# Kernel optimization log

Hardware: AMD Instinct MI355X
Metric: run time of the kernel (lower is better)

Reference implementation:

```python
import jax, jax.numpy as jnp
import numpy as np
import math

N = 4; H = 8; D = 512; DH = D // H; T = 512
MEM = 512; CMEM = 128; RATIO = 4; DFF = 2048; VOCAB = 32000; B = 8
EPS = 1e-5


def _ln(x, g, b):
    mu = x.mean(-1, keepdims=True)
    var = ((x - mu) ** 2).mean(-1, keepdims=True)
    return (x - mu) / jnp.sqrt(var + EPS) * g + b


def _heads(x):
    b, l, _ = x.shape
    return x.reshape(b, l, H, DH).transpose(0, 2, 1, 3)  # [b,h,l,dh]


def _full_attn(q, k, v):
    dots = jnp.einsum('bhid,bhjd->bhij', q, k) * DH ** -0.5
    return jnp.einsum('bhij,bhjd->bhid', jax.nn.softmax(dots, -1), v)


def _pe(t):
    pos = jnp.arange(t, dtype=jnp.float32)[:, None]
    div = jnp.exp(jnp.arange(0, D, 2, dtype=jnp.float32) * (-math.log(10000.0) / D))
    ang = pos * div
    return jnp.stack([jnp.sin(ang), jnp.cos(ang)], axis=-1).reshape(t, D)


def _layer(x, mem, cmem, mask, p):
    (g1, b1, wq, wkv, wo, bo, cw, cb, dw, db, g2, b2, w1, bb1, w2, bb2) = p
    b = x.shape[0]
    y = _ln(x, g1, b1)                       # PreNorm
    q = _heads(y @ wq)
    kv_in = jnp.concatenate([cmem, mem, y], axis=1)
    k, v = jnp.split(kv_in @ wkv, 2, axis=-1)
    k, v = _heads(k), _heads(v)
    dots = jnp.einsum('bhid,bhjd->bhij', q, k) * DH ** -0.5
    mem_tot = mem.shape[1] + cmem.shape[1]
    m2 = mask[:, None, :, None] & mask[:, None, None, :]          # [b,1,t,t]
    fmask = jnp.pad(m2, ((0, 0), (0, 0), (0, 0), (mem_tot, 0)), constant_values=True)
    neg = -jnp.finfo(dots.dtype).max
    dots = jnp.where(fmask, dots, neg)
    out = jnp.einsum('bhij,bhjd->bhid', jax.nn.softmax(dots, -1), v)
    out = out.transpose(0, 2, 1, 3).reshape(b, T, D)
    x = x + out @ wo + bo                    # Residual around attn
    # --- FIFO memory update (t == seq_len, calc_memory) ---
    queue = jnp.concatenate([mem, y], axis=1)        # [b, mem+t, d]
    old_mem = jax.lax.stop_gradient(queue[:, :-MEM]) # detached, len % RATIO == 0
    new_mem = queue[:, -MEM:]
    Lold = old_mem.shape[1]
    seg = old_mem.reshape(b, Lold // RATIO, RATIO, D)
    comp = jnp.einsum('blrd,odr->blo', seg, cw) + cb  # Conv1d k=stride=RATIO
    new_cmem = jnp.concatenate([cmem, comp], axis=1)[:, -CMEM:]
    ck, cv = jnp.split(comp @ wkv, 2, axis=-1)
    ck, cv = _heads(ck), _heads(cv)
    kvlen = k.shape[2]
    start = kvlen - min(mem.shape[1], MEM) - T
    end = kvlen - T
    qd = jax.lax.stop_gradient(q)
    okd = jax.lax.stop_gradient(k[:, :, start:end])
    ovd = jax.lax.stop_gradient(v[:, :, start:end])
    aux = jnp.mean((_full_attn(qd, okd, ovd) - _full_attn(qd, ck, cv)) ** 2)
    recon = jnp.einsum('bld,lm->bmd', comp, dw) + db[None, :, None]  # deconv Linear
    cut = min(recon.shape[1], Lold)
    ae = jnp.mean((old_mem[:, :cut] - recon[:, :cut]) ** 2)
    # --- FF (Residual(PreNorm(FeedForward))) ---
    y2 = _ln(x, g2, b2)
    x = x + jax.nn.gelu(y2 @ w1 + bb1, approximate=False) @ w2 + bb2
    return x, new_mem, new_cmem, aux, ae


def reference(seq, mask, mems, cmems, embed, ln1_g, ln1_b, wq, wkv, wo, bo,
              conv_w, conv_b, deconv_w, deconv_b, ln2_g, ln2_b, w1, b1, w2, b2):
    x = embed[seq] + _pe(seq.shape[1])[None]
    attn_l = jnp.float32(0.0)
    ae_l = jnp.float32(0.0)
    nm, nc = [], []
    for i in range(N):
        p = (ln1_g[i], ln1_b[i], wq[i], wkv[i], wo[i], bo[i], conv_w[i], conv_b[i],
             deconv_w[i], deconv_b[i], ln2_g[i], ln2_b[i], w1[i], b1[i], w2[i], b2[i])
        x, m, c, a, e = _layer(x, mems[i], cmems[i], mask, p)
        nm.append(m); nc.append(c)
        attn_l = attn_l + a; ae_l = ae_l + e
    return x, jnp.stack(nm), jnp.stack(nc), attn_l / N, ae_l / N


def setup_inputs() -> dict:
    key = jax.random.key(0)
    ks = jax.random.split(key, 16)
    s = 0.02
    return {
        'seq': jax.random.randint(ks[0], (B, T), 0, VOCAB),
        'mask': jnp.ones((B, T), dtype=bool),
        'mems': jax.random.normal(ks[1], (N, B, MEM, D), jnp.float32),
        'cmems': jax.random.normal(ks[2], (N, B, CMEM, D), jnp.float32),
        'embed': jax.random.normal(ks[3], (VOCAB, D), jnp.float32) * s,
        'ln1_g': jnp.ones((N, D), jnp.float32),
        'ln1_b': jnp.zeros((N, D), jnp.float32),
        'wq': jax.random.normal(ks[4], (N, D, D), jnp.float32) * s,
        'wkv': jax.random.normal(ks[5], (N, D, 2 * D), jnp.float32) * s,
        'wo': jax.random.normal(ks[6], (N, D, D), jnp.float32) * s,
        'bo': jnp.zeros((N, D), jnp.float32),
        'conv_w': jax.random.normal(ks[7], (N, D, D, RATIO), jnp.float32) * s,
        'conv_b': jnp.zeros((N, D), jnp.float32),
        'deconv_w': jax.random.normal(ks[8], (N, MEM // RATIO, MEM), jnp.float32) * s,
        'deconv_b': jnp.zeros((N, MEM), jnp.float32),
        'ln2_g': jnp.ones((N, D), jnp.float32),
        'ln2_b': jnp.zeros((N, D), jnp.float32),
        'w1': jax.random.normal(ks[9], (N, D, DFF), jnp.float32) * s,
        'b1': jnp.zeros((N, DFF), jnp.float32),
        'w2': jax.random.normal(ks[10], (N, DFF, D), jnp.float32) * s,
        'b2': jnp.zeros((N, D), jnp.float32),
    }
```

## Files before the change

kernel.cpp:

```cpp
#include <hip/hip_runtime.h>
#include <math.h>


#define GBM 128
#define GBN 64
#define GBK 16

template<int EPI>
__global__ __launch_bounds__(256)
void sgemm_k(const float* __restrict__ A, const float* __restrict__ B,
             float* __restrict__ C, const float* __restrict__ bias,
             const float* __restrict__ rbias, const float* __restrict__ ref,
             float* __restrict__ loss,
             int M, int N, int K, int lda, int ldb, int ldc, int ldref,
             long bsA, long bsB, long bsC, long bsRef, int ksplit)
{
    int zb = blockIdx.z;
    int batch = zb / ksplit;
    int ks = zb % ksplit;
    A += (long)batch * bsA;
    B += (long)batch * bsB;
    C += (long)batch * bsC;
    const float* refp = (EPI == 2) ? ref + (long)batch * bsRef : nullptr;

    int m0 = blockIdx.y * GBM;
    int n0 = blockIdx.x * GBN;
    int t = threadIdx.x;
    int tx = t & 15, ty = t >> 4;

    __shared__ float As[GBK][GBM + 4];
    __shared__ float Bs[GBK][GBN];
    __shared__ float red[4];

    float acc[8][4];
#pragma unroll
    for (int i = 0; i < 8; ++i)
#pragma unroll
        for (int j = 0; j < 4; ++j) acc[i][j] = 0.f;

    int arow = t >> 1, acol = (t & 1) * 8;
    int brow = t >> 4, bcol = (t & 15) * 4;

    int kchunk = K / ksplit;
    int kbeg = ks * kchunk, kend = kbeg + kchunk;

    const float* Aptr = A + (long)(m0 + arow) * lda + acol;
    const float* Bptr = B + n0 + bcol;

    for (int k0 = kbeg; k0 < kend; k0 += GBK) {
        float4 a0 = *(const float4*)(Aptr + k0);
        float4 a1 = *(const float4*)(Aptr + k0 + 4);
        float4 b0 = *(const float4*)(Bptr + (long)(k0 + brow) * ldb);
        __syncthreads();
        As[acol + 0][arow] = a0.x;
        As[acol + 1][arow] = a0.y;
        As[acol + 2][arow] = a0.z;
        As[acol + 3][arow] = a0.w;
        As[acol + 4][arow] = a1.x;
        As[acol + 5][arow] = a1.y;
        As[acol + 6][arow] = a1.z;
        As[acol + 7][arow] = a1.w;
        *(float4*)&Bs[brow][bcol] = b0;
        __syncthreads();
#pragma unroll
        for (int kk = 0; kk < GBK; ++kk) {
            float af[8], bf[4];
            *(float4*)&af[0] = *(const float4*)&As[kk][ty * 8];
            *(float4*)&af[4] = *(const float4*)&As[kk][ty * 8 + 4];
            *(float4*)&bf[0] = *(const float4*)&Bs[kk][tx * 4];
#pragma unroll
            for (int i = 0; i < 8; ++i)
#pragma unroll
                for (int j = 0; j < 4; ++j)
                    acc[i][j] = fmaf(af[i], bf[j], acc[i][j]);
        }
    }

    float bv[4] = {0.f, 0.f, 0.f, 0.f};
    if (EPI != 4 && EPI != 2 && bias) *(float4*)bv = *(const float4*)&bias[n0 + tx * 4];

    float lsum = 0.f;
#pragma unroll
    for (int i = 0; i < 8; ++i) {
        int row = m0 + ty * 8 + i;
        float rb = 0.f;
        if (EPI == 2 && rbias) rb = rbias[row];
        float v[4];
#pragma unroll
        for (int j = 0; j < 4; ++j) v[j] = acc[i][j] + bv[j] + rb;
        if (EPI == 0) {
            *(float4*)&C[(long)row * ldc + n0 + tx * 4] = *(float4*)v;
        } else if (EPI == 1) {
            float* cp = &C[(long)row * ldc + n0 + tx * 4];
            float4 old = *(float4*)cp;
            v[0] += old.x; v[1] += old.y; v[2] += old.z; v[3] += old.w;
            *(float4*)cp = *(float4*)v;
        } else if (EPI == 2) {
            const float* rp = &refp[(long)row * ldref + n0 + tx * 4];
#pragma unroll
            for (int j = 0; j < 4; ++j) { float d = v[j] - rp[j]; lsum += d * d; }
        } else if (EPI == 3) {
#pragma unroll
            for (int j = 0; j < 4; ++j)
                v[j] = 0.5f * v[j] * (1.f + erff(v[j] * 0.70710678118654752f));
            *(float4*)&C[(long)row * ldc + n0 + tx * 4] = *(float4*)v;
        } else if (EPI == 4) {
            float* cp = &C[(long)row * ldc + n0 + tx * 4];
#pragma unroll
            for (int j = 0; j < 4; ++j) atomicAdd(cp + j, v[j]);
        }
    }

    if (EPI == 2) {
#pragma unroll
        for (int off = 1; off < 64; off <<= 1) lsum += __shfl_xor(lsum, off);
        if ((t & 63) == 0) red[t >> 6] = lsum;
        __syncthreads();
        if (t == 0) atomicAdd(loss, red[0] + red[1] + red[2] + red[3]);
    }
}

__global__ __launch_bounds__(256)
void attn_k(const float* __restrict__ Q, long qbs,
            const float* __restrict__ K, int ldk, long kbs,
            const float* __restrict__ V, int ldv, long vbs,
            float* __restrict__ O, long obs,
            int Lk, float scale)
{
    int b = blockIdx.z, h = blockIdx.y;
    int lane = threadIdx.x & 63;
    int wv = threadIdx.x >> 6;
    int rw = lane >> 3, g = lane & 7;
    int qrow = blockIdx.x * 32 + wv * 8 + rw;

    const float* qp = Q + (long)b * qbs + (long)qrow * 512 + h * 64 + g * 8;
    float qreg[8];
    *(float4*)&qreg[0] = *(const float4*)qp;
    *(float4*)&qreg[4] = *(const float4*)(qp + 4);

    const float* Kb = K + (long)b * kbs + h * 64;
    const float* Vb = V + (long)b * vbs + h * 64;

    __shared__ float Ks[32][64];
    __shared__ float Vs[32][64];

    int jl = threadIdx.x >> 3;
    int cc = (threadIdx.x & 7) * 8;

    float m = -INFINITY, l = 0.f;
    float acc[8] = {0.f, 0.f, 0.f, 0.f, 0.f, 0.f, 0.f, 0.f};

    for (int j0 = 0; j0 < Lk; j0 += 32) {
        const float* kp = Kb + (long)(j0 + jl) * ldk + cc;
        const float* vp = Vb + (long)(j0 + jl) * ldv + cc;
        float4 k0 = *(const float4*)kp;
        float4 k1 = *(const float4*)(kp + 4);
        float4 v0 = *(const float4*)vp;
        float4 v1 = *(const float4*)(vp + 4);
        __syncthreads();
        *(float4*)&Ks[jl][cc] = k0;
        *(float4*)&Ks[jl][cc + 4] = k1;
        *(float4*)&Vs[jl][cc] = v0;
        *(float4*)&Vs[jl][cc + 4] = v1;
        __syncthreads();
#pragma unroll 8
        for (int jj = 0; jj < 32; ++jj) {
            float4 ka = *(const float4*)&Ks[jj][g * 8];
            float4 kb = *(const float4*)&Ks[jj][g * 8 + 4];
            float p = qreg[0] * ka.x + qreg[1] * ka.y + qreg[2] * ka.z + qreg[3] * ka.w
                    + qreg[4] * kb.x + qreg[5] * kb.y + qreg[6] * kb.z + qreg[7] * kb.w;
            p += __shfl_xor(p, 1);
            p += __shfl_xor(p, 2);
            p += __shfl_xor(p, 4);
            float s = p * scale;
            float mn = fmaxf(m, s);
            float cf = __expf(m - mn);
            float pr = __expf(s - mn);
            l = l * cf + pr;
            m = mn;
            float4 va = *(const float4*)&Vs[jj][g * 8];
            float4 vb = *(const float4*)&Vs[jj][g * 8 + 4];
            acc[0] = acc[0] * cf + pr * va.x;
            acc[1] = acc[1] * cf + pr * va.y;
            acc[2] = acc[2] * cf + pr * va.z;
            acc[3] = acc[3] * cf + pr * va.w;
            acc[4] = acc[4] * cf + pr * vb.x;
            acc[5] = acc[5] * cf + pr * vb.y;
            acc[6] = acc[6] * cf + pr * vb.z;
            acc[7] = acc[7] * cf + pr * vb.w;
        }
    }
    float inv = 1.f / l;
    float* op = O + (long)b * obs + (long)qrow * 512 + h * 64 + g * 8;
    *(float4*)op = make_float4(acc[0] * inv, acc[1] * inv, acc[2] * inv, acc[3] * inv);
    *(float4*)(op + 4) = make_float4(acc[4] * inv, acc[5] * inv, acc[6] * inv, acc[7] * inv);
}

__global__ __launch_bounds__(256)
void ln_k(const float* __restrict__ x, const float* __restrict__ g,
          const float* __restrict__ b, float* __restrict__ y)
{
    int lane = threadIdx.x & 63;
    int row = blockIdx.x * 4 + (threadIdx.x >> 6);
    const float* xr = x + (long)row * 512 + lane * 8;
    float v[8];
    *(float4*)&v[0] = *(const float4*)xr;
    *(float4*)&v[4] = *(const float4*)(xr + 4);
    float s = 0.f, s2 = 0.f;
#pragma unroll
    for (int i = 0; i < 8; ++i) { s += v[i]; s2 += v[i] * v[i]; }
#pragma unroll
    for (int off = 1; off < 64; off <<= 1) {
        s += __shfl_xor(s, off);
        s2 += __shfl_xor(s2, off);
    }
    float mu = s * (1.f / 512.f);
    float var = s2 * (1.f / 512.f) - mu * mu;
    float rstd = rsqrtf(var + 1e-5f);
    float gg[8], bb[8];
    const float* gp = g + lane * 8;
    const float* bp = b + lane * 8;
    *(float4*)&gg[0] = *(const float4*)gp;
    *(float4*)&gg[4] = *(const float4*)(gp + 4);
    *(float4*)&bb[0] = *(const float4*)bp;
    *(float4*)&bb[4] = *(const float4*)(bp + 4);
    float o[8];
#pragma unroll
    for (int i = 0; i < 8; ++i) o[i] = (v[i] - mu) * rstd * gg[i] + bb[i];
    float* yr = y + (long)row * 512 + lane * 8;
    *(float4*)yr = *(float4*)&o[0];
    *(float4*)(yr + 4) = *(float4*)&o[4];
}

__global__ void embed_pe_k(const int* __restrict__ seq, const float* __restrict__ embed,
                           float* __restrict__ X, int total)
{
    int idx = blockIdx.x * 256 + threadIdx.x;
    if (idx >= total) return;
    int d = idx & 511;
    int bt = idx >> 9;
    int tpos = bt & 511;
    int tok = seq[bt];
    float div = __expf(-(float)(d & ~1) * (9.21034037197618f / 512.f));
    float ang = (float)tpos * div;
    float pe = (d & 1) ? cosf(ang) : sinf(ang);
    X[idx] = embed[(long)tok * 512 + d] + pe;
}

__global__ void transpose_cw_k(const float* __restrict__ cw, float* __restrict__ cwT, int total)
{
    int idx = blockIdx.x * 256 + threadIdx.x;
    if (idx >= total) return;
    int r = idx & 3;
    int d = (idx >> 2) & 511;
    int o = (idx >> 11) & 511;
    int L = idx >> 20;
    cwT[(long)L * 1048576 + (long)(r * 512 + d) * 512 + o] = cw[idx];
}
__global__ void transpose_dw_k(const float* __restrict__ dw, float* __restrict__ dwT, int total)
{
    int idx = blockIdx.x * 256 + threadIdx.x;
    if (idx >= total) return;
    int m = idx & 511;
    int j = (idx >> 9) & 127;
    int L = idx >> 16;
    dwT[(long)L * 65536 + m * 128 + j] = dw[idx];
}

__global__ void bias_bcast_k(float* __restrict__ C, const float* __restrict__ bias, int total)
{
    int i = blockIdx.x * 256 + threadIdx.x;
    if (i < total) C[i] = bias[i & 511];
}

__global__ void sqdiff_k(const float* __restrict__ a, const float* __restrict__ b,
                         float* __restrict__ loss, int n4)
{
    __shared__ float red[4];
    int i = blockIdx.x * 256 + threadIdx.x;
    float lsum = 0.f;
    if (i < n4) {
        float4 x = ((const float4*)a)[i];
        float4 y = ((const float4*)b)[i];
        float d0 = x.x - y.x, d1 = x.y - y.y, d2 = x.z - y.z, d3 = x.w - y.w;
        lsum = d0 * d0 + d1 * d1 + d2 * d2 + d3 * d3;
    }
#pragma unroll
    for (int off = 1; off < 64; off <<= 1) lsum += __shfl_xor(lsum, off);
    if ((threadIdx.x & 63) == 0) red[threadIdx.x >> 6] = lsum;
    __syncthreads();
    if (threadIdx.x == 0) atomicAdd(loss, red[0] + red[1] + red[2] + red[3]);
}

__global__ void zero_loss_k(float* loss)
{
    if (threadIdx.x < 8) loss[threadIdx.x] = 0.f;
}

__global__ void finalize_k(const float* __restrict__ loss, float* __restrict__ out)
{
    if (threadIdx.x == 0) out[0] = loss[0] * (1.f / (4.f * 2097152.f));
    if (threadIdx.x == 1) out[1] = loss[1] * (1.f / (4.f * 2097152.f));
}

static void gemm(hipStream_t st, int EPI, const float* A, const float* B, float* C,
                 const float* bias, const float* rbias, const float* ref, float* loss,
                 int M, int N, int K, int lda, int ldb, int ldc, int ldref,
                 long bsA, long bsB, long bsC, long bsRef, int batches, int ksplit)
{
    dim3 g(N / GBN, M / GBM, batches * ksplit), blk(256);
    switch (EPI) {
    case 0: sgemm_k<0><<<g, blk, 0, st>>>(A, B, C, bias, rbias, ref, loss, M, N, K, lda, ldb, ldc, ldref, bsA, bsB, bsC, bsRef, ksplit); break;
    case 1: sgemm_k<1><<<g, blk, 0, st>>>(A, B, C, bias, rbias, ref, loss, M, N, K, lda, ldb, ldc, ldref, bsA, bsB, bsC, bsRef, ksplit); break;
    case 2: sgemm_k<2><<<g, blk, 0, st>>>(A, B, C, bias, rbias, ref, loss, M, N, K, lda, ldb, ldc, ldref, bsA, bsB, bsC, bsRef, ksplit); break;
    case 3: sgemm_k<3><<<g, blk, 0, st>>>(A, B, C, bias, rbias, ref, loss, M, N, K, lda, ldb, ldc, ldref, bsA, bsB, bsC, bsRef, ksplit); break;
    case 4: sgemm_k<4><<<g, blk, 0, st>>>(A, B, C, bias, rbias, ref, loss, M, N, K, lda, ldb, ldc, ldref, bsA, bsB, bsC, bsRef, ksplit); break;
    }
}

static void attn(hipStream_t st, const float* Q, long qbs, const float* K, int ldk, long kbs,
                 const float* V, int ldv, long vbs, float* O, long obs, int Lk)
{
    dim3 g(16, 8, 8), blk(256);
    attn_k<<<g, blk, 0, st>>>(Q, qbs, K, ldk, kbs, V, ldv, vbs, O, obs, Lk, 0.125f);
}

extern "C" void kernel_launch(void* const* d_in, const int* in_sizes, int n_in,
                              void* d_out, int out_size, void* d_ws, size_t ws_size,
                              hipStream_t stream)
{
    const int*   seq     = (const int*)d_in[0];
    const float* mems    = (const float*)d_in[2];
    const float* cmems   = (const float*)d_in[3];
    const float* embed   = (const float*)d_in[4];
    const float* ln1_g   = (const float*)d_in[5];
    const float* ln1_b   = (const float*)d_in[6];
    const float* wq      = (const float*)d_in[7];
    const float* wkv     = (const float*)d_in[8];
    const float* wo      = (const float*)d_in[9];
    const float* bo      = (const float*)d_in[10];
    const float* conv_w  = (const float*)d_in[11];
    const float* conv_b  = (const float*)d_in[12];
    const float* deconv_w= (const float*)d_in[13];
    const float* deconv_b= (const float*)d_in[14];
    const float* ln2_g   = (const float*)d_in[15];
    const float* ln2_b   = (const float*)d_in[16];
    const float* w1      = (const float*)d_in[17];
    const float* b1      = (const float*)d_in[18];
    const float* w2      = (const float*)d_in[19];
    const float* b2      = (const float*)d_in[20];

    float* out = (float*)d_out;
    float* X      = out;
    float* nm_out = out + 2097152;
    float* nc_out = out + 2097152 + 8388608;
    float* sc_out = out + 12582912;

    float* ws = (float*)d_ws;
    float* Qb   = ws;
    float* KV   = ws + 2097152;
    float* ATTN = ws + 11534336;
    float* FFN1 = ws + 13631488;
    float* CWT  = ws + 22020096;
    float* DWT  = ws + 26214400;
    float* LOSS = ws + 26476544;
    float* Y2   = Qb;
    float* CKV  = ATTN;
    float* AUX1 = FFN1;
    float* AUX2 = FFN1 + 2097152;

    zero_loss_k<<<1, 64, 0, stream>>>(LOSS);
    transpose_cw_k<<<16384, 256, 0, stream>>>(conv_w, CWT, 4194304);
    transpose_dw_k<<<1024, 256, 0, stream>>>(deconv_w, DWT, 262144);
    embed_pe_k<<<8192, 256, 0, stream>>>(seq, embed, X, 2097152);

    for (int L = 0; L < 4; ++L) {
        const float* mem_l  = mems  + (long)L * 2097152;
        const float* cmem_l = cmems + (long)L * 524288;
        float* y_l    = nm_out + (long)L * 2097152;
        float* comp_l = nc_out + (long)L * 524288;
        const float* wq_l  = wq  + (long)L * 262144;
        const float* wkv_l = wkv + (long)L * 524288;
        const float* wo_l  = wo  + (long)L * 262144;
        const float* bo_l  = bo  + L * 512;
        const float* cb_l  = conv_b + L * 512;
        const float* db_l  = deconv_b + L * 512;
        const float* w1_l  = w1 + (long)L * 1048576;
        const float* bb1_l = b1 + L * 2048;
        const float* w2_l  = w2 + (long)L * 1048576;
        const float* bb2_l = b2 + L * 512;
        const float* cwT_l = CWT + (long)L * 1048576;
        const float* dwT_l = DWT + (long)L * 65536;

        ln_k<<<1024, 256, 0, stream>>>(X, ln1_g + L * 512, ln1_b + L * 512, y_l);

        gemm(stream, 0, y_l, wq_l, Qb, nullptr, nullptr, nullptr, nullptr,
             4096, 512, 512, 512, 512, 512, 0, 0, 0, 0, 0, 1, 1);

        gemm(stream, 0, cmem_l, wkv_l, KV, nullptr, nullptr, nullptr, nullptr,
             128, 1024, 512, 512, 1024, 1024, 0, 65536, 0, 1179648, 0, 8, 1);
        gemm(stream, 0, mem_l, wkv_l, KV + 131072, nullptr, nullptr, nullptr, nullptr,
             512, 1024, 512, 512, 1024, 1024, 0, 262144, 0, 1179648, 0, 8, 1);
        gemm(stream, 0, y_l, wkv_l, KV + 655360, nullptr, nullptr, nullptr, nullptr,
             512, 1024, 512, 512, 1024, 1024, 0, 262144, 0, 1179648, 0, 8, 1);

        attn(stream, Qb, 262144, KV, 1024, 1179648, KV + 512, 1024, 1179648,
             ATTN, 262144, 1152);

        gemm(stream, 1, ATTN, wo_l, X, bo_l, nullptr, nullptr, nullptr,
             4096, 512, 512, 512, 512, 512, 0, 0, 0, 0, 0, 1, 1);

        bias_bcast_k<<<2048, 256, 0, stream>>>(comp_l, cb_l, 524288);
        gemm(stream, 4, mem_l, cwT_l, comp_l, nullptr, nullptr, nullptr, nullptr,
             1024, 512, 2048, 2048, 512, 512, 0, 0, 0, 0, 0, 1, 4);

        gemm(stream, 0, comp_l, wkv_l, CKV, nullptr, nullptr, nullptr, nullptr,
             1024, 1024, 512, 512, 1024, 1024, 0, 0, 0, 0, 0, 1, 1);

        attn(stream, Qb, 262144, KV + 131072, 1024, 1179648, KV + 131584, 1024, 1179648,
             AUX1, 262144, 512);
        attn(stream, Qb, 262144, CKV, 1024, 131072, CKV + 512, 1024, 131072,
             AUX2, 262144, 128);
        sqdiff_k<<<2048, 256, 0, stream>>>(AUX1, AUX2, LOSS + 0, 524288);

        gemm(stream, 2, dwT_l, comp_l, nullptr, nullptr, db_l, mem_l, LOSS + 1,
             512, 512, 128, 128, 512, 0, 512, 0, 65536, 0, 262144, 8, 1);

        ln_k<<<1024, 256, 0, stream>>>(X, ln2_g + L * 512, ln2_b + L * 512, Y2);
        gemm(stream, 3, Y2, w1_l, FFN1, bb1_l, nullptr, nullptr, nullptr,
             4096, 2048, 512, 512, 2048, 2048, 0, 0, 0, 0, 0, 1, 1);
        gemm(stream, 1, FFN1, w2_l, X, bb2_l, nullptr, nullptr, nullptr,
             4096, 512, 2048, 2048, 512, 512, 0, 0, 0, 0, 0, 1, 1);
    }

    finalize_k<<<1, 64, 0, stream>>>(LOSS, sc_out);
}
```

Baseline: 5.685 ms.

## Fuse KV projections, block-wise softmax attention, fused aux loss, split-K residual GEMMs

```diff
diff --git a/kernel.cpp b/kernel.cpp
--- a/kernel.cpp
+++ b/kernel.cpp
@@ -47,10 +47,11 @@
     const float* Aptr = A + (long)(m0 + arow) * lda + acol;
     const float* Bptr = B + n0 + bcol;
 
+    float4 a0 = *(const float4*)(Aptr + kbeg);
+    float4 a1 = *(const float4*)(Aptr + kbeg + 4);
+    float4 b0 = *(const float4*)(Bptr + (long)(kbeg + brow) * ldb);
+
     for (int k0 = kbeg; k0 < kend; k0 += GBK) {
-        float4 a0 = *(const float4*)(Aptr + k0);
-        float4 a1 = *(const float4*)(Aptr + k0 + 4);
-        float4 b0 = *(const float4*)(Bptr + (long)(k0 + brow) * ldb);
         __syncthreads();
         As[acol + 0][arow] = a0.x;
         As[acol + 1][arow] = a0.y;
@@ -62,6 +63,12 @@
         As[acol + 7][arow] = a1.w;
         *(float4*)&Bs[brow][bcol] = b0;
         __syncthreads();
+
+        int kn = (k0 + GBK < kend) ? k0 + GBK : kbeg;
+        float4 na0 = *(const float4*)(Aptr + kn);
+        float4 na1 = *(const float4*)(Aptr + kn + 4);
+        float4 nb0 = *(const float4*)(Bptr + (long)(kn + brow) * ldb);
+
 #pragma unroll
         for (int kk = 0; kk < GBK; ++kk) {
             float af[8], bf[4];
@@ -74,10 +81,16 @@
                 for (int j = 0; j < 4; ++j)
                     acc[i][j] = fmaf(af[i], bf[j], acc[i][j]);
         }
+        a0 = na0; a1 = na1; b0 = nb0;
     }
 
     float bv[4] = {0.f, 0.f, 0.f, 0.f};
     if (EPI != 4 && EPI != 2 && bias) *(float4*)bv = *(const float4*)&bias[n0 + tx * 4];
+    if (EPI == 5) {
+        float inv = 1.f / (float)ksplit;
+#pragma unroll
+        for (int j = 0; j < 4; ++j) bv[j] *= inv;
+    }
 
     float lsum = 0.f;
 #pragma unroll
@@ -104,7 +117,7 @@
             for (int j = 0; j < 4; ++j)
                 v[j] = 0.5f * v[j] * (1.f + erff(v[j] * 0.70710678118654752f));
             *(float4*)&C[(long)row * ldc + n0 + tx * 4] = *(float4*)v;
-        } else if (EPI == 4) {
+        } else if (EPI == 4 || EPI == 5) {
             float* cp = &C[(long)row * ldc + n0 + tx * 4];
 #pragma unroll
             for (int j = 0; j < 4; ++j) atomicAdd(cp + j, v[j]);
@@ -120,36 +133,13 @@
     }
 }
 
-__global__ __launch_bounds__(256)
-void attn_k(const float* __restrict__ Q, long qbs,
-            const float* __restrict__ K, int ldk, long kbs,
-            const float* __restrict__ V, int ldv, long vbs,
-            float* __restrict__ O, long obs,
-            int Lk, float scale)
-{
-    int b = blockIdx.z, h = blockIdx.y;
-    int lane = threadIdx.x & 63;
-    int wv = threadIdx.x >> 6;
-    int rw = lane >> 3, g = lane & 7;
-    int qrow = blockIdx.x * 32 + wv * 8 + rw;
-
-    const float* qp = Q + (long)b * qbs + (long)qrow * 512 + h * 64 + g * 8;
-    float qreg[8];
-    *(float4*)&qreg[0] = *(const float4*)qp;
-    *(float4*)&qreg[4] = *(const float4*)(qp + 4);
-
-    const float* Kb = K + (long)b * kbs + h * 64;
-    const float* Vb = V + (long)b * vbs + h * 64;
-
-    __shared__ float Ks[32][64];
-    __shared__ float Vs[32][64];
-
-    int jl = threadIdx.x >> 3;
-    int cc = (threadIdx.x & 7) * 8;
-
-    float m = -INFINITY, l = 0.f;
-    float acc[8] = {0.f, 0.f, 0.f, 0.f, 0.f, 0.f, 0.f, 0.f};
-
+#define LKP 68
+
+__device__ __forceinline__ void attn_core(
+    const float* __restrict__ Kb, int ldk, const float* __restrict__ Vb, int ldv,
+    int Lk, const float q[8], int jl, int cc, int g,
+    float (&Ks)[32][LKP], float (&Vs)[32][LKP], float acc[8], float& m, float& l)
+{
     for (int j0 = 0; j0 < Lk; j0 += 32) {
         const float* kp = Kb + (long)(j0 + jl) * ldk + cc;
         const float* vp = Vb + (long)(j0 + jl) * ldv + cc;
@@ -163,42 +153,120 @@
         *(float4*)&Vs[jl][cc] = v0;
         *(float4*)&Vs[jl][cc + 4] = v1;
         __syncthreads();
-#pragma unroll 8
+
+        float s[32];
+#pragma unroll
         for (int jj = 0; jj < 32; ++jj) {
             float4 ka = *(const float4*)&Ks[jj][g * 8];
             float4 kb = *(const float4*)&Ks[jj][g * 8 + 4];
-            float p = qreg[0] * ka.x + qreg[1] * ka.y + qreg[2] * ka.z + qreg[3] * ka.w
-                    + qreg[4] * kb.x + qreg[5] * kb.y + qreg[6] * kb.z + qreg[7] * kb.w;
+            float p = q[0] * ka.x + q[1] * ka.y + q[2] * ka.z + q[3] * ka.w
+                    + q[4] * kb.x + q[5] * kb.y + q[6] * kb.z + q[7] * kb.w;
             p += __shfl_xor(p, 1);
             p += __shfl_xor(p, 2);
             p += __shfl_xor(p, 4);
-            float s = p * scale;
-            float mn = fmaxf(m, s);
-            float cf = __expf(m - mn);
-            float pr = __expf(s - mn);
-            l = l * cf + pr;
-            m = mn;
+            s[jj] = p;
+        }
+        float tm = s[0];
+#pragma unroll
+        for (int jj = 1; jj < 32; ++jj) tm = fmaxf(tm, s[jj]);
+        float mn = fmaxf(m, tm);
+        float cf = __builtin_exp2f(m - mn);
+        m = mn;
+        l *= cf;
+#pragma unroll
+        for (int i = 0; i < 8; ++i) acc[i] *= cf;
+#pragma unroll
+        for (int jj = 0; jj < 32; ++jj) {
+            float pr = __builtin_exp2f(s[jj] - mn);
+            l += pr;
             float4 va = *(const float4*)&Vs[jj][g * 8];
             float4 vb = *(const float4*)&Vs[jj][g * 8 + 4];
-            acc[0] = acc[0] * cf + pr * va.x;
-            acc[1] = acc[1] * cf + pr * va.y;
-            acc[2] = acc[2] * cf + pr * va.z;
-            acc[3] = acc[3] * cf + pr * va.w;
-            acc[4] = acc[4] * cf + pr * vb.x;
-            acc[5] = acc[5] * cf + pr * vb.y;
-            acc[6] = acc[6] * cf + pr * vb.z;
-            acc[7] = acc[7] * cf + pr * vb.w;
+            acc[0] = fmaf(pr, va.x, acc[0]);
+            acc[1] = fmaf(pr, va.y, acc[1]);
+            acc[2] = fmaf(pr, va.z, acc[2]);
+            acc[3] = fmaf(pr, va.w, acc[3]);
+            acc[4] = fmaf(pr, vb.x, acc[4]);
+            acc[5] = fmaf(pr, vb.y, acc[5]);
+            acc[6] = fmaf(pr, vb.z, acc[6]);
+            acc[7] = fmaf(pr, vb.w, acc[7]);
         }
     }
+}
+
+#define ATTN_PRE()                                                        \
+    int b = blockIdx.z, h = blockIdx.y;                                   \
+    int lane = threadIdx.x & 63;                                          \
+    int wv = threadIdx.x >> 6;                                            \
+    int rw = lane >> 3, g = lane & 7;                                     \
+    int qrow = blockIdx.x * 32 + wv * 8 + rw;                             \
+    int jl = threadIdx.x >> 3, cc = (threadIdx.x & 7) * 8;                \
+    const float* qp = Q + (long)b * 262144 + (long)qrow * 512 + h * 64 + g * 8; \
+    float q[8];                                                           \
+    *(float4*)&q[0] = *(const float4*)qp;                                 \
+    *(float4*)&q[4] = *(const float4*)(qp + 4);                           \
+    const float kSc = 0.125f * 1.44269504088896f;                         \
+    _Pragma("unroll") for (int i = 0; i < 8; ++i) q[i] *= kSc;
+
+__global__ __launch_bounds__(256)
+void attn_k(const float* __restrict__ Q,
+            const float* __restrict__ K, int ldk, long kbs,
+            const float* __restrict__ V, int ldv, long vbs,
+            float* __restrict__ O, int Lk)
+{
+    ATTN_PRE();
+    __shared__ float Ks[32][LKP];
+    __shared__ float Vs[32][LKP];
+    float m = -1e30f, l = 0.f;
+    float acc[8] = {0.f, 0.f, 0.f, 0.f, 0.f, 0.f, 0.f, 0.f};
+    attn_core(K + (long)b * kbs + h * 64, ldk, V + (long)b * vbs + h * 64, ldv,
+              Lk, q, jl, cc, g, Ks, Vs, acc, m, l);
     float inv = 1.f / l;
-    float* op = O + (long)b * obs + (long)qrow * 512 + h * 64 + g * 8;
+    float* op = O + (long)b * 262144 + (long)qrow * 512 + h * 64 + g * 8;
     *(float4*)op = make_float4(acc[0] * inv, acc[1] * inv, acc[2] * inv, acc[3] * inv);
     *(float4*)(op + 4) = make_float4(acc[4] * inv, acc[5] * inv, acc[6] * inv, acc[7] * inv);
 }
 
 __global__ __launch_bounds__(256)
+void aux_k(const float* __restrict__ Q,
+           const float* __restrict__ K1, int ldk1, long kbs1,
+           const float* __restrict__ V1, int ldv1, long vbs1, int Lk1,
+           const float* __restrict__ K2, int ldk2, long kbs2,
+           const float* __restrict__ V2, int ldv2, long vbs2, int Lk2,
+           float* __restrict__ loss)
+{
+    ATTN_PRE();
+    __shared__ float Ks[32][LKP];
+    __shared__ float Vs[32][LKP];
+    __shared__ float red[4];
+    float m = -1e30f, l = 0.f;
+    float acc[8] = {0.f, 0.f, 0.f, 0.f, 0.f, 0.f, 0.f, 0.f};
+    attn_core(K1 + (long)b * kbs1 + h * 64, ldk1, V1 + (long)b * vbs1 + h * 64, ldv1,
+              Lk1, q, jl, cc, g, Ks, Vs, acc, m, l);
+    float inv = 1.f / l;
+    float o1[8];
+#pragma unroll
+    for (int i = 0; i < 8; ++i) o1[i] = acc[i] * inv;
+
+    m = -1e30f; l = 0.f;
+#pragma unroll
+    for (int i = 0; i < 8; ++i) acc[i] = 0.f;
+    attn_core(K2 + (long)b * kbs2 + h * 64, ldk2, V2 + (long)b * vbs2 + h * 64, ldv2,
+              Lk2, q, jl, cc, g, Ks, Vs, acc, m, l);
+    inv = 1.f / l;
+    float lsum = 0.f;
+#pragma unroll
+    for (int i = 0; i < 8; ++i) { float d = o1[i] - acc[i] * inv; lsum += d * d; }
+#pragma unroll
+    for (int off = 1; off < 64; off <<= 1) lsum += __shfl_xor(lsum, off);
+    if ((threadIdx.x & 63) == 0) red[threadIdx.x >> 6] = lsum;
+    __syncthreads();
+    if (threadIdx.x == 0) atomicAdd(loss, red[0] + red[1] + red[2] + red[3]);
+}
+
+__global__ __launch_bounds__(256)
 void ln_k(const float* __restrict__ x, const float* __restrict__ g,
-          const float* __restrict__ b, float* __restrict__ y)
+          const float* __restrict__ b, float* __restrict__ y,
+          float* __restrict__ y2)
 {
     int lane = threadIdx.x & 63;
     int row = blockIdx.x * 4 + (threadIdx.x >> 6);
@@ -218,18 +286,36 @@
     float var = s2 * (1.f / 512.f) - mu * mu;
     float rstd = rsqrtf(var + 1e-5f);
     float gg[8], bb[8];
-    const float* gp = g + lane * 8;
-    const float* bp = b + lane * 8;
-    *(float4*)&gg[0] = *(const float4*)gp;
-    *(float4*)&gg[4] = *(const float4*)(gp + 4);
-    *(float4*)&bb[0] = *(const float4*)bp;
-    *(float4*)&bb[4] = *(const float4*)(bp + 4);
+    *(float4*)&gg[0] = *(const float4*)(g + lane * 8);
+    *(float4*)&gg[4] = *(const float4*)(g + lane * 8 + 4);
+    *(float4*)&bb[0] = *(const float4*)(b + lane * 8);
+    *(float4*)&bb[4] = *(const float4*)(b + lane * 8 + 4);
     float o[8];
 #pragma unroll
     for (int i = 0; i < 8; ++i) o[i] = (v[i] - mu) * rstd * gg[i] + bb[i];
     float* yr = y + (long)row * 512 + lane * 8;
     *(float4*)yr = *(float4*)&o[0];
     *(float4*)(yr + 4) = *(float4*)&o[4];
+    if (y2) {
+        long crow = (long)(row >> 9) * 1152 + 640 + (row & 511);
+        float* yr2 = y2 + crow * 512 + lane * 8;
+        *(float4*)yr2 = *(float4*)&o[0];
+        *(float4*)(yr2 + 4) = *(float4*)&o[4];
+    }
+}
+
+__global__ void cat_k(const float4* __restrict__ cmem, const float4* __restrict__ mem,
+                      float4* __restrict__ CAT)
+{
+    int i = blockIdx.x * 256 + threadIdx.x;
+    if (i >= 655360) return;
+    int b = i / 81920;
+    int rem = i - b * 81920;
+    int r = rem >> 7;
+    int c = rem & 127;
+    float4 v = (r < 128) ? cmem[((long)b * 128 + r) * 128 + c]
+                         : mem[((long)b * 512 + (r - 128)) * 128 + c];
+    CAT[((long)b * 1152 + r) * 128 + c] = v;
 }
 
 __global__ void embed_pe_k(const int* __restrict__ seq, const float* __restrict__ embed,
@@ -273,25 +359,6 @@
     if (i < total) C[i] = bias[i & 511];
 }
 
-__global__ void sqdiff_k(const float* __restrict__ a, const float* __restrict__ b,
-                         float* __restrict__ loss, int n4)
-{
-    __shared__ float red[4];
-    int i = blockIdx.x * 256 + threadIdx.x;
-    float lsum = 0.f;
-    if (i < n4) {
-        float4 x = ((const float4*)a)[i];
-        float4 y = ((const float4*)b)[i];
-        float d0 = x.x - y.x, d1 = x.y - y.y, d2 = x.z - y.z, d3 = x.w - y.w;
-        lsum = d0 * d0 + d1 * d1 + d2 * d2 + d3 * d3;
-    }
-#pragma unroll
-    for (int off = 1; off < 64; off <<= 1) lsum += __shfl_xor(lsum, off);
-    if ((threadIdx.x & 63) == 0) red[threadIdx.x >> 6] = lsum;
-    __syncthreads();
-    if (threadIdx.x == 0) atomicAdd(loss, red[0] + red[1] + red[2] + red[3]);
-}
-
 __global__ void zero_loss_k(float* loss)
 {
     if (threadIdx.x < 8) loss[threadIdx.x] = 0.f;
@@ -315,14 +382,8 @@
     case 2: sgemm_k<2><<<g, blk, 0, st>>>(A, B, C, bias, rbias, ref, loss, M, N, K, lda, ldb, ldc, ldref, bsA, bsB, bsC, bsRef, ksplit); break;
     case 3: sgemm_k<3><<<g, blk, 0, st>>>(A, B, C, bias, rbias, ref, loss, M, N, K, lda, ldb, ldc, ldref, bsA, bsB, bsC, bsRef, ksplit); break;
     case 4: sgemm_k<4><<<g, blk, 0, st>>>(A, B, C, bias, rbias, ref, loss, M, N, K, lda, ldb, ldc, ldref, bsA, bsB, bsC, bsRef, ksplit); break;
-    }
-}
-
-static void attn(hipStream_t st, const float* Q, long qbs, const float* K, int ldk, long kbs,
-                 const float* V, int ldv, long vbs, float* O, long obs, int Lk)
-{
-    dim3 g(16, 8, 8), blk(256);
-    attn_k<<<g, blk, 0, st>>>(Q, qbs, K, ldk, kbs, V, ldv, vbs, O, obs, Lk, 0.125f);
+    case 5: sgemm_k<5><<<g, blk, 0, st>>>(A, B, C, bias, rbias, ref, loss, M, N, K, lda, ldb, ldc, ldref, bsA, bsB, bsC, bsRef, ksplit); break;
+    }
 }
 
 extern "C" void kernel_launch(void* const* d_in, const int* in_sizes, int n_in,
@@ -356,18 +417,18 @@
     float* nc_out = out + 2097152 + 8388608;
     float* sc_out = out + 12582912;
 
-    float* ws = (float*)d_ws;
-    float* Qb   = ws;
-    float* KV   = ws + 2097152;
+    float* ws   = (float*)d_ws;
+    float* KVQ  = ws;
+    float* Qb   = ws + 9437184;
     float* ATTN = ws + 11534336;
-    float* FFN1 = ws + 13631488;
+    float* SH   = ws + 13631488;
     float* CWT  = ws + 22020096;
     float* DWT  = ws + 26214400;
     float* LOSS = ws + 26476544;
     float* Y2   = Qb;
     float* CKV  = ATTN;
-    float* AUX1 = FFN1;
-    float* AUX2 = FFN1 + 2097152;
+    float* CAT  = SH;
+    float* FFN1 = SH;
 
     zero_loss_k<<<1, 64, 0, stream>>>(LOSS);
     transpose_cw_k<<<16384, 256, 0, stream>>>(conv_w, CWT, 4194304);
@@ -392,23 +453,24 @@
         const float* cwT_l = CWT + (long)L * 1048576;
         const float* dwT_l = DWT + (long)L * 65536;
 
-        ln_k<<<1024, 256, 0, stream>>>(X, ln1_g + L * 512, ln1_b + L * 512, y_l);
+        ln_k<<<1024, 256, 0, stream>>>(X, ln1_g + L * 512, ln1_b + L * 512, y_l, CAT);
+        cat_k<<<2560, 256, 0, stream>>>((const float4*)cmem_l, (const float4*)mem_l,
+                                        (float4*)CAT);
+
+        gemm(stream, 0, CAT, wkv_l, KVQ, nullptr, nullptr, nullptr, nullptr,
+             9216, 1024, 512, 512, 1024, 1024, 0, 0, 0, 0, 0, 1, 1);
 
         gemm(stream, 0, y_l, wq_l, Qb, nullptr, nullptr, nullptr, nullptr,
              4096, 512, 512, 512, 512, 512, 0, 0, 0, 0, 0, 1, 1);
 
-        gemm(stream, 0, cmem_l, wkv_l, KV, nullptr, nullptr, nullptr, nullptr,
-             128, 1024, 512, 512, 1024, 1024, 0, 65536, 0, 1179648, 0, 8, 1);
-        gemm(stream, 0, mem_l, wkv_l, KV + 131072, nullptr, nullptr, nullptr, nullptr,
-             512, 1024, 512, 512, 1024, 1024, 0, 262144, 0, 1179648, 0, 8, 1);
-        gemm(stream, 0, y_l, wkv_l, KV + 655360, nullptr, nullptr, nullptr, nullptr,
-             512, 1024, 512, 512, 1024, 1024, 0, 262144, 0, 1179648, 0, 8, 1);
-
-        attn(stream, Qb, 262144, KV, 1024, 1179648, KV + 512, 1024, 1179648,
-             ATTN, 262144, 1152);
-
-        gemm(stream, 1, ATTN, wo_l, X, bo_l, nullptr, nullptr, nullptr,
-             4096, 512, 512, 512, 512, 512, 0, 0, 0, 0, 0, 1, 1);
+        {
+            dim3 g(16, 8, 8), blk(256);
+            attn_k<<<g, blk, 0, stream>>>(Qb, KVQ, 1024, 1179648,
+                                          KVQ + 512, 1024, 1179648, ATTN, 1152);
+        }
+
+        gemm(stream, 5, ATTN, wo_l, X, bo_l, nullptr, nullptr, nullptr,
+             4096, 512, 512, 512, 512, 512, 0, 0, 0, 0, 0, 1, 2);
 
         bias_bcast_k<<<2048, 256, 0, stream>>>(comp_l, cb_l, 524288);
         gemm(stream, 4, mem_l, cwT_l, comp_l, nullptr, nullptr, nullptr, nullptr,
@@ -417,20 +479,22 @@
         gemm(stream, 0, comp_l, wkv_l, CKV, nullptr, nullptr, nullptr, nullptr,
              1024, 1024, 512, 512, 1024, 1024, 0, 0, 0, 0, 0, 1, 1);
 
-        attn(stream, Qb, 262144, KV + 131072, 1024, 1179648, KV + 131584, 1024, 1179648,
-             AUX1, 262144, 512);
-        attn(stream, Qb, 262144, CKV, 1024, 131072, CKV + 512, 1024, 131072,
-             AUX2, 262144, 128);
-        sqdiff_k<<<2048, 256, 0, stream>>>(AUX1, AUX2, LOSS + 0, 524288);
+        {
+            dim3 g(16, 8, 8), blk(256);
+            aux_k<<<g, blk, 0, stream>>>(Qb,
+                KVQ + 131072, 1024, 1179648, KVQ + 131584, 1024, 1179648, 512,
+                CKV, 1024, 131072, CKV + 512, 1024, 131072, 128,
+                LOSS + 0);
+        }
 
         gemm(stream, 2, dwT_l, comp_l, nullptr, nullptr, db_l, mem_l, LOSS + 1,
              512, 512, 128, 128, 512, 0, 512, 0, 65536, 0, 262144, 8, 1);
 
-        ln_k<<<1024, 256, 0, stream>>>(X, ln2_g + L * 512, ln2_b + L * 512, Y2);
+        ln_k<<<1024, 256, 0, stream>>>(X, ln2_g + L * 512, ln2_b + L * 512, Y2, nullptr);
         gemm(stream, 3, Y2, w1_l, FFN1, bb1_l, nullptr, nullptr, nullptr,
              4096, 2048, 512, 512, 2048, 2048, 0, 0, 0, 0, 0, 1, 1);
-        gemm(stream, 1, FFN1, w2_l, X, bb2_l, nullptr, nullptr, nullptr,
-             4096, 512, 2048, 2048, 512, 512, 0, 0, 0, 0, 0, 1, 1);
+        gemm(stream, 5, FFN1, w2_l, X, bb2_l, nullptr, nullptr, nullptr,
+             4096, 512, 2048, 2048, 512, 512, 0, 0, 0, 0, 0, 1, 2);
     }
 
     finalize_k<<<1, 64, 0, stream>>>(LOSS, sc_out);
```

Result: no change. 5.758 ms (+1.3%).
